# Kernel tuning notes

Measured on AMD Instinct MI355X. Metric: run time of the kernel, lower is better.

Reference implementation:

```python
import jax, jax.numpy as jnp
import numpy as np
import math

D_MODEL = 1024
N_HEADS = 16
D_HEAD = 64
D_MLP = 4096
N_LAYERS = 12
INIT_STD = 0.02
EPS = 1e-5
BATCH = 2
SEQ = 2048


def setup_inputs() -> dict:
    key = jax.random.key(0)
    ks = jax.random.split(key, 8)
    attn_std = INIT_STD
    proj_std = INIT_STD / math.sqrt(2 * N_LAYERS)
    return {
        "resid_pre": jax.random.normal(ks[0], (BATCH, SEQ, D_MODEL), jnp.float32),
        "ln1_w": jnp.ones((D_MODEL,), jnp.float32),
        "ln1_b": jnp.zeros((D_MODEL,), jnp.float32),
        "W_Q": attn_std * jax.random.normal(ks[1], (N_HEADS, D_MODEL, D_HEAD), jnp.float32),
        "b_Q": jnp.zeros((N_HEADS, D_HEAD), jnp.float32),
        "W_K": attn_std * jax.random.normal(ks[2], (N_HEADS, D_MODEL, D_HEAD), jnp.float32),
        "b_K": jnp.zeros((N_HEADS, D_HEAD), jnp.float32),
        "W_V": attn_std * jax.random.normal(ks[3], (N_HEADS, D_MODEL, D_HEAD), jnp.float32),
        "b_V": jnp.zeros((N_HEADS, D_HEAD), jnp.float32),
        "W_O": proj_std * jax.random.normal(ks[4], (N_HEADS, D_HEAD, D_MODEL), jnp.float32),
        "b_O": jnp.zeros((D_MODEL,), jnp.float32),
        "ln2_w": jnp.ones((D_MODEL,), jnp.float32),
        "ln2_b": jnp.zeros((D_MODEL,), jnp.float32),
        "W_in": INIT_STD * jax.random.normal(ks[5], (D_MODEL, D_MLP), jnp.float32),
        "b_in": jnp.zeros((D_MLP,), jnp.float32),
        "W_out": proj_std * jax.random.normal(ks[6], (D_MLP, D_MODEL), jnp.float32),
        "b_out": jnp.zeros((D_MODEL,), jnp.float32),
    }


def _layernorm(x, w, b):
    mean = x.mean(-1, keepdims=True)
    var = x.var(-1, keepdims=True)  # unbiased=False
    return (x - mean) / jnp.sqrt(var + EPS) * w + b


def _attention(x, W_Q, b_Q, W_K, b_K, W_V, b_V, W_O, b_O):
    # x: [b, s, d]; W_*: [h, d, k]
    q = jnp.einsum('bsd,hdk->bshk', x, W_Q) + b_Q
    k = jnp.einsum('bsd,hdk->bshk', x, W_K) + b_K
    v = jnp.einsum('bsd,hdk->bshk', x, W_V) + b_V
    scores = jnp.einsum('bqhk,bshk->bhqs', q, k) / math.sqrt(D_HEAD)
    seq = x.shape[1]
    causal = jnp.tril(jnp.ones((seq, seq), bool))
    scores = jnp.where(causal, scores, -jnp.inf)
    pattern = jax.nn.softmax(scores, axis=-1)
    z = jnp.einsum('bhqs,bshk->bqhk', pattern, v)
    return jnp.einsum('bqhk,hkd->bqd', z, W_O) + b_O


def reference(resid_pre, ln1_w, ln1_b, W_Q, b_Q, W_K, b_K, W_V, b_V, W_O, b_O,
              ln2_w, ln2_b, W_in, b_in, W_out, b_out):
    attn_out = _attention(_layernorm(resid_pre, ln1_w, ln1_b),
                          W_Q, b_Q, W_K, b_K, W_V, b_V, W_O, b_O)
    resid_mid = resid_pre + attn_out
    h = _layernorm(resid_mid, ln2_w, ln2_b)
    mlp_out = jnp.matmul(jax.nn.relu(jnp.matmul(h, W_in) + b_in), W_out) + b_out
    return resid_mid + mlp_out
```

## Files before the change

kernel.cpp:

```cpp
#include <hip/hip_runtime.h>
#include <stdint.h>


typedef unsigned short u16;
typedef __bf16 bf16x8 __attribute__((ext_vector_type(8)));
typedef __bf16 bf16x4 __attribute__((ext_vector_type(4)));
typedef short  s16x4  __attribute__((ext_vector_type(4)));
typedef float  f32x4  __attribute__((ext_vector_type(4)));

#define QSCALE 0.18033688011112042f

__device__ __forceinline__ float bf2f(unsigned int u) {
  union { unsigned int u; float f; } v; v.u = u << 16; return v.f;
}
__device__ __forceinline__ u16 f2bf(float f) {
  union { float f; unsigned int u; } v; v.f = f;
  unsigned int r = v.u + 0x7FFFu + ((v.u >> 16) & 1u);
  return (u16)(r >> 16);
}
__device__ __forceinline__ float loadf(const void* p, size_t i, int isf) {
  return isf ? ((const float*)p)[i] : bf2f(((const u16*)p)[i]);
}

typedef const __attribute__((address_space(1))) void* gas_t;
typedef __attribute__((address_space(3))) void* las_t;
__device__ __forceinline__ void gl_lds16(const u16* g, u16* l) {
  __builtin_amdgcn_global_load_lds((gas_t)g, (las_t)l, 16, 0, 0);
}

__device__ __forceinline__ f32x4 mfma16(s16x4 a, s16x4 b, f32x4 c) {
#if __has_builtin(__builtin_amdgcn_mfma_f32_16x16x16_bf16)
  return __builtin_amdgcn_mfma_f32_16x16x16_bf16(
      __builtin_bit_cast(bf16x4, a), __builtin_bit_cast(bf16x4, b), c, 0, 0, 0);
#else
  return __builtin_amdgcn_mfma_f32_16x16x16bf16_1k(a, b, c, 0, 0, 0);
#endif
}

__global__ __launch_bounds__(256) void detect_dtype(
    const unsigned int* __restrict__ x, int* __restrict__ flag) {
  __shared__ int cnt;
  if (threadIdx.x == 0) cnt = 0;
  __syncthreads();
  int c = 0;
  for (int i = threadIdx.x; i < 512; i += 256) {
    unsigned int e = (x[i] >> 23) & 0xFFu;
    if (e >= 97u && e <= 157u) c++;
  }
  atomicAdd(&cnt, c);
  __syncthreads();
  if (threadIdx.x == 0) *flag = (cnt > 384) ? 1 : 0;
}

__global__ __launch_bounds__(256) void pack_qkv_tiled(
    const int* __restrict__ flagp,
    const void* __restrict__ Wq, const void* __restrict__ Wk, const void* __restrict__ Wv,
    u16* __restrict__ WT) {
  __shared__ float t[64][65];
  const int isf = *flagp;
  const int tid = threadIdx.x;
  const int mh = blockIdx.y;
  const int mat = mh >> 4, h = mh & 15;
  const int d0 = blockIdx.x << 6;
  const void* src = (mat == 0) ? Wq : (mat == 1) ? Wk : Wv;
  const float scale = (mat == 0) ? QSCALE : 1.f;
  const int lane = tid & 63, rr = tid >> 6;
  const size_t sbase = ((size_t)h << 16) + lane;
#pragma unroll
  for (int i = 0; i < 16; i++) {
    int d = i * 4 + rr;
    t[d][lane] = loadf(src, sbase + (size_t)(d0 + d) * 64, isf) * scale;
  }
  __syncthreads();
#pragma unroll
  for (int i = 0; i < 16; i++) {
    int k = i * 4 + rr;
    WT[((size_t)((mat << 10) + (h << 6) + k) << 10) + d0 + lane] = f2bf(t[lane][k]);
  }
}

__global__ __launch_bounds__(256) void transpose_tiled(
    const int* __restrict__ flagp, const void* __restrict__ src,
    u16* __restrict__ dst, int R, int C) {
  __shared__ float t[64][65];
  const int isf = *flagp;
  const int tid = threadIdx.x;
  const int c0 = blockIdx.x << 6, r0 = blockIdx.y << 6;
  const int lane = tid & 63, rr = tid >> 6;
#pragma unroll
  for (int i = 0; i < 16; i++) {
    int r = i * 4 + rr;
    t[r][lane] = loadf(src, (size_t)(r0 + r) * C + c0 + lane, isf);
  }
  __syncthreads();
#pragma unroll
  for (int i = 0; i < 16; i++) {
    int c = i * 4 + rr;
    dst[(size_t)(c0 + c) * R + r0 + lane] = f2bf(t[lane][c]);
  }
}

__global__ __launch_bounds__(256) void pack_biases(
    const int* __restrict__ flagp,
    const void* bq, const void* bk, const void* bv,
    const void* bO, const void* bin, const void* bout,
    float* __restrict__ out) {
  const int isf = *flagp;
  int i = blockIdx.x * 256 + threadIdx.x;
  float v;
  if (i < 1024)      v = loadf(bq,   i,        isf) * QSCALE;
  else if (i < 2048) v = loadf(bk,   i - 1024, isf);
  else if (i < 3072) v = loadf(bv,   i - 2048, isf);
  else if (i < 4096) v = loadf(bO,   i - 3072, isf);
  else if (i < 8192) v = loadf(bin,  i - 4096, isf);
  else               v = loadf(bout, i - 8192, isf);
  out[i] = v;
}

template<int SRC>
__global__ __launch_bounds__(256) void ln_fwd(
    const int* __restrict__ flagp, const void* __restrict__ xin,
    const void* __restrict__ w, const void* __restrict__ b,
    u16* __restrict__ out) {
  const int isf = *flagp;
  const int row = blockIdx.x, tid = threadIdx.x;
  const int col = tid << 2;
  const size_t base = ((size_t)row << 10) + col;
  float v[4];
#pragma unroll
  for (int i = 0; i < 4; i++)
    v[i] = (SRC == 1) ? ((const float*)xin)[base + i] : loadf(xin, base + i, isf);
  float s  = v[0] + v[1] + v[2] + v[3];
  float ss = v[0]*v[0] + v[1]*v[1] + v[2]*v[2] + v[3]*v[3];
#pragma unroll
  for (int mk = 32; mk >= 1; mk >>= 1) {
    s  += __shfl_xor(s,  mk, 64);
    ss += __shfl_xor(ss, mk, 64);
  }
  __shared__ float red[8];
  if ((tid & 63) == 0) { red[tid >> 6] = s; red[4 + (tid >> 6)] = ss; }
  __syncthreads();
  float S  = red[0] + red[1] + red[2] + red[3];
  float SS = red[4] + red[5] + red[6] + red[7];
  float mean = S * (1.f / 1024.f);
  float var  = SS * (1.f / 1024.f) - mean * mean;
  float rstd = rsqrtf(var + 1e-5f);
  u16 e[4];
#pragma unroll
  for (int i = 0; i < 4; i++) {
    float wv = loadf(w, col + i, isf);
    float bv = loadf(b, col + i, isf);
    e[i] = f2bf((v[i] - mean) * rstd * wv + bv);
  }
  uint2 o;
  o.x = (unsigned)e[0] | ((unsigned)e[1] << 16);
  o.y = (unsigned)e[2] | ((unsigned)e[3] << 16);
  *(uint2*)(out + base) = o;
}

template<int MODE, int TM>
__global__ __launch_bounds__(256) void gemm_bt(
    const int* __restrict__ flagp,
    const u16* __restrict__ A, const u16* __restrict__ BT,
    const float* __restrict__ bias, const void* __restrict__ resid,
    void* __restrict__ out, void* __restrict__ out2, void* __restrict__ out3,
    int M, int N, int K, int SHL) {
  constexpr int WR = TM / 32;
  __shared__ u16 as[TM * 32];
  __shared__ u16 bs[128 * 32];
  int isf = 0;
  if (MODE == 2 || MODE == 3) isf = *flagp;
  const int Lb = blockIdx.x;
  const int xcd = Lb & 7, sidx = Lb >> 3;
  const int SH = 1 << SHL;
  const int by = xcd * SH + (sidx & (SH - 1));
  const int bx = sidx >> SHL;
  const int tid = threadIdx.x;
  const int L = tid & 63, w = tid >> 6;
  const int wm = (w >> 1) * (TM >> 1), wn = (w & 1) << 6;
  const int row0 = by * TM, col0 = bx << 7;
  const int m = L & 15, quad = L >> 4;

  f32x4 zero4 = {0.f, 0.f, 0.f, 0.f};
  f32x4 acc[WR][4];
#pragma unroll
  for (int i = 0; i < WR; i++)
#pragma unroll
    for (int j = 0; j < 4; j++) acc[i][j] = zero4;

  const int tm = tid >> 2;
  const int tk = (tid & 3) << 3;
  const u16* Ag  = A  + (size_t)(row0 + tm) * K + tk;
  const u16* Ag2 = Ag + (size_t)64 * K;
  const u16* Bg  = BT + (size_t)(col0 + tm) * K + tk;
  const u16* Bg2 = Bg + (size_t)64 * K;
  u16* asl  = &as[tid * 8];
  u16* asl2 = &as[2048 + tid * 8];
  u16* bsl  = &bs[tid * 8];
  u16* bsl2 = &bs[2048 + tid * 8];

  const int aoff = (wm + m) * 32 + quad * 8;
  const int boff = (wn + m) * 32 + quad * 8;

  for (int kk = 0; kk < K; kk += 32) {
    __syncthreads();
    gl_lds16(Ag + kk, asl);
    if (TM == 128) gl_lds16(Ag2 + kk, asl2);
    gl_lds16(Bg + kk, bsl);
    gl_lds16(Bg2 + kk, bsl2);
    __syncthreads();
    bf16x8 af[WR], bfr[4];
#pragma unroll
    for (int i = 0; i < WR; i++) af[i]  = *(const bf16x8*)&as[aoff + i * 512];
#pragma unroll
    for (int j = 0; j < 4; j++) bfr[j] = *(const bf16x8*)&bs[boff + j * 512];
#pragma unroll
    for (int i = 0; i < WR; i++)
#pragma unroll
      for (int j = 0; j < 4; j++)
        acc[i][j] = __builtin_amdgcn_mfma_f32_16x16x32_bf16(af[i], bfr[j], acc[i][j], 0, 0, 0);
  }

#pragma unroll
  for (int j = 0; j < 4; j++) {
    const int col = col0 + wn + j * 16 + m;
    const float bval = bias[col];
    if (MODE == 4) {
      const int sel = col >> 10;
      const int hh  = (col >> 6) & 15;
      const int f   = col & 63;
#pragma unroll
      for (int i = 0; i < WR; i++) {
        const int rowb = row0 + wm + i * 16 + quad * 4;
        if (sel < 2) {
          u16* dst = (u16*)(sel ? out2 : out);
#pragma unroll
          for (int r = 0; r < 4; r++)
            dst[((((size_t)hh << 12) + rowb + r) << 6) + f] = f2bf(acc[i][j][r] + bval);
        } else {
          u16 e[4];
#pragma unroll
          for (int r = 0; r < 4; r++) e[r] = f2bf(acc[i][j][r] + bval);
          uint2 o;
          o.x = (unsigned)e[0] | ((unsigned)e[1] << 16);
          o.y = (unsigned)e[2] | ((unsigned)e[3] << 16);
          *(uint2*)&((u16*)out3)[(((size_t)hh * 64 + f) << 12) + rowb] = o;
        }
      }
    } else {
#pragma unroll
      for (int i = 0; i < WR; i++) {
        const int rowb = row0 + wm + i * 16 + quad * 4;
#pragma unroll
        for (int r = 0; r < 4; r++) {
          float vv = acc[i][j][r] + bval;
          size_t idx = (size_t)(rowb + r) * N + col;
          if (MODE == 1) {
            ((u16*)out)[idx] = f2bf(fmaxf(vv, 0.f));
          } else if (MODE == 2) {
            ((float*)out)[idx] = vv + loadf(resid, idx, isf);
          } else if (MODE == 3) {
            float o = vv + ((const float*)resid)[idx];
            if (isf) ((float*)out)[idx] = o;
            else     ((u16*)out)[idx]   = f2bf(o);
          }
        }
      }
    }
  }
}

__global__ __launch_bounds__(256, 3) void attn_part(
    const u16* __restrict__ qh, const u16* __restrict__ kh,
    const u16* __restrict__ vT, u16* __restrict__ Opart,
    float* __restrict__ stats) {
  const int combo = blockIdx.x;
  const int qt = blockIdx.y;
  const int ci = blockIdx.z;
  const int q0 = qt << 6;
  const int nc = (q0 + 64 + 511) >> 9;
  if (ci >= nc) return;
  const int k_lo = ci << 9;
  const int k_hi = min(k_lo + 512, q0 + 64);
  const int nsteps = (k_hi - k_lo + 127) >> 7;

  __shared__ u16 kS[128 * 72];
  __shared__ u16 vS[64 * 136];
  const int tid = threadIdx.x, L = tid & 63, w = tid >> 6;
  const int m = L & 15, quad = L >> 4;
  const int h = combo >> 1, b = combo & 1;
  const size_t tb = (size_t)b * 2048;
  const size_t hbase = (size_t)h * 4096;
  const int qg = q0 + w * 16 + m;

  s16x4 qf[4];
  {
    const u16* qp = qh + ((hbase + tb + (size_t)(q0 + w * 16 + m)) << 6) + quad * 4;
#pragma unroll
    for (int fg = 0; fg < 4; fg++) qf[fg] = *(const s16x4*)(qp + fg * 16);
  }
  const s16x4 ones = {(short)0x3F80, (short)0x3F80, (short)0x3F80, (short)0x3F80};

  f32x4 zero4 = {0.f, 0.f, 0.f, 0.f};
  f32x4 O[4];
#pragma unroll
  for (int ft = 0; ft < 4; ft++) O[ft] = zero4;
  f32x4 lacc = zero4;
  float mrow = -30000.f;

  const int krow[4] = { (0*256+tid) >> 3, (1*256+tid) >> 3, (2*256+tid) >> 3, (3*256+tid) >> 3 };
  const int kc = tid & 7;
  const int vf[4] = { (0*256+tid) >> 4, (1*256+tid) >> 4, (2*256+tid) >> 4, (3*256+tid) >> 4 };
  const int vc = tid & 15;

  int4 kr[4], vr[4];
#pragma unroll
  for (int i = 0; i < 4; i++) {
    kr[i] = *(const int4*)(kh + ((hbase + tb + k_lo + krow[i]) << 6) + kc * 8);
    vr[i] = *(const int4*)(vT + (((size_t)h * 64 + vf[i]) << 12) + tb + k_lo + vc * 8);
  }

  for (int j = 0; j < nsteps; j++) {
    const int k0 = k_lo + (j << 7);
    __syncthreads();
#pragma unroll
    for (int i = 0; i < 4; i++) {
      *(int4*)&kS[krow[i] * 72 + kc * 8] = kr[i];
      *(int4*)&vS[vf[i] * 136 + vc * 8] = vr[i];
    }
    __syncthreads();
    if (j + 1 < nsteps) {
      const int k1 = k_lo + ((j + 1) << 7);
#pragma unroll
      for (int i = 0; i < 4; i++) {
        kr[i] = *(const int4*)(kh + ((hbase + tb + k1 + krow[i]) << 6) + kc * 8);
        vr[i] = *(const int4*)(vT + (((size_t)h * 64 + vf[i]) << 12) + tb + k1 + vc * 8);
      }
    }
    f32x4 sc[8];
#pragma unroll
    for (int kt = 0; kt < 8; kt++) {
      f32x4 t = zero4;
#pragma unroll
      for (int fg = 0; fg < 4; fg++) {
        s16x4 ka = *(const s16x4*)&kS[(kt * 16 + m) * 72 + fg * 16 + quad * 4];
        t = mfma16(ka, qf[fg], t);
      }
      sc[kt] = t;
    }
    if (k0 + 128 > q0) {
#pragma unroll
      for (int kt = 0; kt < 8; kt++)
#pragma unroll
        for (int r = 0; r < 4; r++) {
          int ktok = k0 + kt * 16 + quad * 4 + r;
          if (ktok > qg) sc[kt][r] = -30000.f;
        }
    }
    float mx = sc[0][0];
#pragma unroll
    for (int kt = 0; kt < 8; kt++)
#pragma unroll
      for (int r = 0; r < 4; r++) mx = fmaxf(mx, sc[kt][r]);
    mx = fmaxf(mx, __shfl_xor(mx, 16, 64));
    mx = fmaxf(mx, __shfl_xor(mx, 32, 64));
    float mnew = fmaxf(mrow, mx);
    float alpha = __builtin_amdgcn_exp2f(mrow - mnew);
    mrow = mnew;
#pragma unroll
    for (int ft = 0; ft < 4; ft++) O[ft] *= alpha;
    lacc *= alpha;
    s16x4 pb[8];
#pragma unroll
    for (int kt = 0; kt < 8; kt++)
#pragma unroll
      for (int r = 0; r < 4; r++)
        pb[kt][r] = (short)f2bf(__builtin_amdgcn_exp2f(sc[kt][r] - mnew));
#pragma unroll
    for (int kt = 0; kt < 8; kt++) {
      lacc = mfma16(ones, pb[kt], lacc);
#pragma unroll
      for (int ft = 0; ft < 4; ft++) {
        s16x4 va = *(const s16x4*)&vS[(ft * 16 + m) * 136 + kt * 16 + quad * 4];
        O[ft] = mfma16(va, pb[kt], O[ft]);
      }
    }
  }

  __syncthreads();
#pragma unroll
  for (int ft = 0; ft < 4; ft++) {
    s16x4 o4;
#pragma unroll
    for (int r = 0; r < 4; r++) o4[r] = (short)f2bf(O[ft][r]);
    *(s16x4*)&kS[(w * 16 + m) * 72 + ft * 16 + quad * 4] = o4;
  }
  __syncthreads();
  const int slot = (combo * 32 + qt) * 4 + ci;
  u16* op = Opart + ((size_t)slot << 12);
#pragma unroll
  for (int it = 0; it < 2; it++) {
    int idx = it * 256 + tid;
    int row = idx >> 3, c = idx & 7;
    *(int4*)&op[row * 64 + c * 8] = *(const int4*)&kS[row * 72 + c * 8];
  }
  if (quad == 0) {
    stats[slot * 128 + w * 16 + m]      = mrow;
    stats[slot * 128 + 64 + w * 16 + m] = lacc[0];
  }
}

__global__ __launch_bounds__(256) void attn_merge(
    const u16* __restrict__ Opart, const float* __restrict__ stats,
    u16* __restrict__ z) {
  const int combo = blockIdx.x, qt = blockIdx.y;
  const int h = combo >> 1, b = combo & 1;
  const int q0 = qt << 6;
  const int nc = (q0 + 64 + 511) >> 9;
  const int tid = threadIdx.x;
  const int t = tid >> 2, f0 = (tid & 3) << 4;
  const int slot0 = (combo * 32 + qt) * 4;
  float M = -3e4f;
  for (int ci = 0; ci < nc; ci++)
    M = fmaxf(M, stats[(slot0 + ci) * 128 + t]);
  float acc[16];
#pragma unroll
  for (int e = 0; e < 16; e++) acc[e] = 0.f;
  float ltot = 0.f;
  for (int ci = 0; ci < nc; ci++) {
    float mi = stats[(slot0 + ci) * 128 + t];
    float li = stats[(slot0 + ci) * 128 + 64 + t];
    float wgt = exp2f(mi - M);
    ltot += wgt * li;
    const u16* op = Opart + (((size_t)(slot0 + ci)) << 12) + t * 64 + f0;
    union { int4 v; u16 u[8]; } a0, a1;
    a0.v = *(const int4*)op;
    a1.v = *(const int4*)(op + 8);
#pragma unroll
    for (int e = 0; e < 8; e++) {
      acc[e]     += wgt * bf2f(a0.u[e]);
      acc[8 + e] += wgt * bf2f(a1.u[e]);
    }
  }
  float inv = 1.f / ltot;
  union { int4 v; u16 u[8]; } o0, o1;
#pragma unroll
  for (int e = 0; e < 8; e++) {
    o0.u[e] = f2bf(acc[e] * inv);
    o1.u[e] = f2bf(acc[8 + e] * inv);
  }
  size_t tok = (size_t)b * 2048 + q0 + t;
  *(int4*)&z[tok * 1024 + h * 64 + f0]     = o0.v;
  *(int4*)&z[tok * 1024 + h * 64 + f0 + 8] = o1.v;
}

extern "C" void kernel_launch(void* const* d_in, const int* in_sizes, int n_in,
                              void* d_out, int out_size, void* d_ws, size_t ws_size,
                              hipStream_t stream) {
  (void)in_sizes; (void)n_in; (void)out_size; (void)ws_size;
  const void* resid_pre = d_in[0];
  const void* ln1_w = d_in[1];
  const void* ln1_b = d_in[2];
  const void* W_Q   = d_in[3];
  const void* b_Q   = d_in[4];
  const void* W_K   = d_in[5];
  const void* b_K   = d_in[6];
  const void* W_V   = d_in[7];
  const void* b_V   = d_in[8];
  const void* W_O   = d_in[9];
  const void* b_O   = d_in[10];
  const void* ln2_w = d_in[11];
  const void* ln2_b = d_in[12];
  const void* W_in  = d_in[13];
  const void* b_in  = d_in[14];
  const void* W_out = d_in[15];
  const void* b_out = d_in[16];

  char* p = (char*)d_ws;
  auto alloc = [&](size_t bytes) {
    char* r = p; p += (bytes + 255) & ~(size_t)255; return (void*)r;
  };
  int*   flag      = (int*)  alloc(256);
  u16*   WqkvT     = (u16*)  alloc(3072ull * 1024 * 2);
  u16*   WoT       = (u16*)  alloc(1024ull * 1024 * 2);
  u16*   WinT      = (u16*)  alloc(4096ull * 1024 * 2);
  u16*   WoutT     = (u16*)  alloc(1024ull * 4096 * 2);
  float* biases    = (float*)alloc(9216 * 4);
  u16*   xn        = (u16*)  alloc(4096ull * 1024 * 2);
  u16*   q_hm      = (u16*)  alloc(16ull * 4096 * 64 * 2);
  u16*   k_hm      = (u16*)  alloc(16ull * 4096 * 64 * 2);
  u16*   vTws      = (u16*)  alloc(16ull * 64 * 4096 * 2);
  float* resid_mid = (float*)alloc(4096ull * 1024 * 4);
  u16*   h2        = (u16*)  alloc(4096ull * 1024 * 2);
  u16*   act       = (u16*)  alloc(4096ull * 4096 * 2);
  u16*   z = xn;
  u16*   Opart = act;
  float* stats = (float*)h2;

  detect_dtype<<<1, 256, 0, stream>>>((const unsigned int*)resid_pre, flag);

  pack_qkv_tiled<<<dim3(16, 48), 256, 0, stream>>>(flag, W_Q, W_K, W_V, WqkvT);
  transpose_tiled<<<dim3(16, 16), 256, 0, stream>>>(flag, W_O,   WoT,   1024, 1024);
  transpose_tiled<<<dim3(64, 16), 256, 0, stream>>>(flag, W_in,  WinT,  1024, 4096);
  transpose_tiled<<<dim3(16, 64), 256, 0, stream>>>(flag, W_out, WoutT, 4096, 1024);
  pack_biases<<<36, 256, 0, stream>>>(flag, b_Q, b_K, b_V, b_O, b_in, b_out, biases);

  ln_fwd<0><<<4096, 256, 0, stream>>>(flag, resid_pre, ln1_w, ln1_b, xn);
  gemm_bt<4, 128><<<768, 256, 0, stream>>>(
      flag, xn, WqkvT, biases, nullptr, q_hm, k_hm, vTws, 4096, 3072, 1024, 2);
  attn_part<<<dim3(32, 32, 4), 256, 0, stream>>>(q_hm, k_hm, vTws, Opart, stats);
  attn_merge<<<dim3(32, 32), 256, 0, stream>>>(Opart, stats, z);
  gemm_bt<2, 64><<<512, 256, 0, stream>>>(
      flag, z, WoT, biases + 3072, resid_pre, resid_mid, nullptr, nullptr, 4096, 1024, 1024, 3);
  ln_fwd<1><<<4096, 256, 0, stream>>>(flag, resid_mid, ln2_w, ln2_b, h2);
  gemm_bt<1, 128><<<1024, 256, 0, stream>>>(
      flag, h2, WinT, biases + 4096, nullptr, act, nullptr, nullptr, 4096, 4096, 1024, 2);
  gemm_bt<3, 64><<<512, 256, 0, stream>>>(
      flag, act, WoutT, biases + 8192, resid_mid, d_out, nullptr, nullptr, 4096, 1024, 4096, 3);
}
```

Before: 498.6 us.

## Rework attention MFMA shapes, row-sum, V layout, and GEMM register prefetch

The GEMM drops direct global-to-LDS loads in favour of register double-buffering: the next K tile is fetched into registers while MFMAs run on the current one. The attention QK^T now uses 16x16x32 bf16 MFMAs with 8-wide loads. The row-sum moves from an MFMA against a ones vector to scalar adds plus shuffles. V is stored into LDS with a permuted column layout so PV operands can be read as 8-wide vectors. Float-to-bf16 conversions use the packed hardware convert when available. These changes aim to cut instruction count and LDS traffic, at the cost of more registers and a riskier layout change.

```diff
diff --git a/kernel.cpp b/kernel.cpp
--- a/kernel.cpp
+++ b/kernel.cpp
@@ -5,6 +5,7 @@
 typedef unsigned short u16;
 typedef __bf16 bf16x8 __attribute__((ext_vector_type(8)));
 typedef __bf16 bf16x4 __attribute__((ext_vector_type(4)));
+typedef __bf16 bf16x2 __attribute__((ext_vector_type(2)));
 typedef short  s16x4  __attribute__((ext_vector_type(4)));
 typedef float  f32x4  __attribute__((ext_vector_type(4)));
 
@@ -18,14 +19,16 @@
   unsigned int r = v.u + 0x7FFFu + ((v.u >> 16) & 1u);
   return (u16)(r >> 16);
 }
+__device__ __forceinline__ unsigned pkbf(float lo, float hi) {
+#if __has_builtin(__builtin_amdgcn_cvt_pk_bf16_f32)
+  bf16x2 t = __builtin_amdgcn_cvt_pk_bf16_f32(lo, hi);
+  return __builtin_bit_cast(unsigned, t);
+#else
+  return (unsigned)f2bf(lo) | ((unsigned)f2bf(hi) << 16);
+#endif
+}
 __device__ __forceinline__ float loadf(const void* p, size_t i, int isf) {
   return isf ? ((const float*)p)[i] : bf2f(((const u16*)p)[i]);
-}
-
-typedef const __attribute__((address_space(1))) void* gas_t;
-typedef __attribute__((address_space(3))) void* las_t;
-__device__ __forceinline__ void gl_lds16(const u16* g, u16* l) {
-  __builtin_amdgcn_global_load_lds((gas_t)g, (las_t)l, 16, 0, 0);
 }
 
 __device__ __forceinline__ f32x4 mfma16(s16x4 a, s16x4 b, f32x4 c) {
@@ -202,13 +205,25 @@
   const int aoff = (wm + m) * 32 + quad * 8;
   const int boff = (wn + m) * 32 + quad * 8;
 
+  int4 ar0, ar1, br0, br1;
+  ar0 = *(const int4*)Ag;
+  if (TM == 128) ar1 = *(const int4*)Ag2;
+  br0 = *(const int4*)Bg;
+  br1 = *(const int4*)Bg2;
+
   for (int kk = 0; kk < K; kk += 32) {
     __syncthreads();
-    gl_lds16(Ag + kk, asl);
-    if (TM == 128) gl_lds16(Ag2 + kk, asl2);
-    gl_lds16(Bg + kk, bsl);
-    gl_lds16(Bg2 + kk, bsl2);
+    *(int4*)asl = ar0;
+    if (TM == 128) *(int4*)asl2 = ar1;
+    *(int4*)bsl = br0;
+    *(int4*)bsl2 = br1;
     __syncthreads();
+    if (kk + 32 < K) {
+      ar0 = *(const int4*)(Ag + kk + 32);
+      if (TM == 128) ar1 = *(const int4*)(Ag2 + kk + 32);
+      br0 = *(const int4*)(Bg + kk + 32);
+      br1 = *(const int4*)(Bg2 + kk + 32);
+    }
     bf16x8 af[WR], bfr[4];
 #pragma unroll
     for (int i = 0; i < WR; i++) af[i]  = *(const bf16x8*)&as[aoff + i * 512];
@@ -238,12 +253,9 @@
           for (int r = 0; r < 4; r++)
             dst[((((size_t)hh << 12) + rowb + r) << 6) + f] = f2bf(acc[i][j][r] + bval);
         } else {
-          u16 e[4];
-#pragma unroll
-          for (int r = 0; r < 4; r++) e[r] = f2bf(acc[i][j][r] + bval);
           uint2 o;
-          o.x = (unsigned)e[0] | ((unsigned)e[1] << 16);
-          o.y = (unsigned)e[2] | ((unsigned)e[3] << 16);
+          o.x = pkbf(acc[i][j][0] + bval, acc[i][j][1] + bval);
+          o.y = pkbf(acc[i][j][2] + bval, acc[i][j][3] + bval);
           *(uint2*)&((u16*)out3)[(((size_t)hh * 64 + f) << 12) + rowb] = o;
         }
       }
@@ -293,25 +305,27 @@
   const size_t hbase = (size_t)h * 4096;
   const int qg = q0 + w * 16 + m;
 
-  s16x4 qf[4];
+  bf16x8 qb0, qb1;
   {
-    const u16* qp = qh + ((hbase + tb + (size_t)(q0 + w * 16 + m)) << 6) + quad * 4;
-#pragma unroll
-    for (int fg = 0; fg < 4; fg++) qf[fg] = *(const s16x4*)(qp + fg * 16);
-  }
-  const s16x4 ones = {(short)0x3F80, (short)0x3F80, (short)0x3F80, (short)0x3F80};
+    const u16* qp = qh + ((hbase + tb + (size_t)qg) << 6) + quad * 8;
+    qb0 = *(const bf16x8*)qp;
+    qb1 = *(const bf16x8*)(qp + 32);
+  }
 
   f32x4 zero4 = {0.f, 0.f, 0.f, 0.f};
   f32x4 O[4];
 #pragma unroll
   for (int ft = 0; ft < 4; ft++) O[ft] = zero4;
-  f32x4 lacc = zero4;
-  float mrow = -30000.f;
+  float mrow = -30000.f, lrow = 0.f;
 
   const int krow[4] = { (0*256+tid) >> 3, (1*256+tid) >> 3, (2*256+tid) >> 3, (3*256+tid) >> 3 };
   const int kc = tid & 7;
   const int vf[4] = { (0*256+tid) >> 4, (1*256+tid) >> 4, (2*256+tid) >> 4, (3*256+tid) >> 4 };
   const int vc = tid & 15;
+  const int vq = (vc & 1) << 1;
+  const int vk4 = (vc >> 1) << 2;
+  const int vc0 = (vq << 5) + vk4;
+  const int vc1 = ((vq + 1) << 5) + vk4;
 
   int4 kr[4], vr[4];
 #pragma unroll
@@ -326,7 +340,9 @@
 #pragma unroll
     for (int i = 0; i < 4; i++) {
       *(int4*)&kS[krow[i] * 72 + kc * 8] = kr[i];
-      *(int4*)&vS[vf[i] * 136 + vc * 8] = vr[i];
+      union { int4 v; s16x4 hh[2]; } tv; tv.v = vr[i];
+      *(s16x4*)&vS[vf[i] * 136 + vc0] = tv.hh[0];
+      *(s16x4*)&vS[vf[i] * 136 + vc1] = tv.hh[1];
     }
     __syncthreads();
     if (j + 1 < nsteps) {
@@ -340,12 +356,12 @@
     f32x4 sc[8];
 #pragma unroll
     for (int kt = 0; kt < 8; kt++) {
+      const u16* kp = &kS[(kt * 16 + m) * 72 + quad * 8];
+      bf16x8 ka0 = *(const bf16x8*)kp;
+      bf16x8 ka1 = *(const bf16x8*)(kp + 32);
       f32x4 t = zero4;
-#pragma unroll
-      for (int fg = 0; fg < 4; fg++) {
-        s16x4 ka = *(const s16x4*)&kS[(kt * 16 + m) * 72 + fg * 16 + quad * 4];
-        t = mfma16(ka, qf[fg], t);
-      }
+      t = __builtin_amdgcn_mfma_f32_16x16x32_bf16(ka0, qb0, t, 0, 0, 0);
+      t = __builtin_amdgcn_mfma_f32_16x16x32_bf16(ka1, qb1, t, 0, 0, 0);
       sc[kt] = t;
     }
     if (k0 + 128 > q0) {
@@ -367,22 +383,34 @@
     float mnew = fmaxf(mrow, mx);
     float alpha = __builtin_amdgcn_exp2f(mrow - mnew);
     mrow = mnew;
+    s16x4 pb[8];
+    float sum = 0.f;
+#pragma unroll
+    for (int kt = 0; kt < 8; kt++) {
+      float e0 = __builtin_amdgcn_exp2f(sc[kt][0] - mnew);
+      float e1 = __builtin_amdgcn_exp2f(sc[kt][1] - mnew);
+      float e2 = __builtin_amdgcn_exp2f(sc[kt][2] - mnew);
+      float e3 = __builtin_amdgcn_exp2f(sc[kt][3] - mnew);
+      sum += (e0 + e1) + (e2 + e3);
+      union { uint2 u; s16x4 hh; } pu;
+      pu.u.x = pkbf(e0, e1);
+      pu.u.y = pkbf(e2, e3);
+      pb[kt] = pu.hh;
+    }
+    sum += __shfl_xor(sum, 16, 64);
+    sum += __shfl_xor(sum, 32, 64);
+    lrow = lrow * alpha + sum;
 #pragma unroll
     for (int ft = 0; ft < 4; ft++) O[ft] *= alpha;
-    lacc *= alpha;
-    s16x4 pb[8];
-#pragma unroll
-    for (int kt = 0; kt < 8; kt++)
-#pragma unroll
-      for (int r = 0; r < 4; r++)
-        pb[kt][r] = (short)f2bf(__builtin_amdgcn_exp2f(sc[kt][r] - mnew));
-#pragma unroll
-    for (int kt = 0; kt < 8; kt++) {
-      lacc = mfma16(ones, pb[kt], lacc);
-#pragma unroll
-      for (int ft = 0; ft < 4; ft++) {
-        s16x4 va = *(const s16x4*)&vS[(ft * 16 + m) * 136 + kt * 16 + quad * 4];
-        O[ft] = mfma16(va, pb[kt], O[ft]);
+#pragma unroll
+    for (int ft = 0; ft < 4; ft++) {
+      const u16* vp = &vS[(ft * 16 + m) * 136 + quad * 32];
+#pragma unroll
+      for (int pr = 0; pr < 4; pr++) {
+        union { bf16x8 v; s16x4 hh[2]; } u;
+        u.v = *(const bf16x8*)(vp + pr * 8);
+        O[ft] = mfma16(u.hh[0], pb[2 * pr],     O[ft]);
+        O[ft] = mfma16(u.hh[1], pb[2 * pr + 1], O[ft]);
       }
     }
   }
@@ -390,10 +418,10 @@
   __syncthreads();
 #pragma unroll
   for (int ft = 0; ft < 4; ft++) {
-    s16x4 o4;
-#pragma unroll
-    for (int r = 0; r < 4; r++) o4[r] = (short)f2bf(O[ft][r]);
-    *(s16x4*)&kS[(w * 16 + m) * 72 + ft * 16 + quad * 4] = o4;
+    union { uint2 u; s16x4 hh; } o4;
+    o4.u.x = pkbf(O[ft][0], O[ft][1]);
+    o4.u.y = pkbf(O[ft][2], O[ft][3]);
+    *(s16x4*)&kS[(w * 16 + m) * 72 + ft * 16 + quad * 4] = o4.hh;
   }
   __syncthreads();
   const int slot = (combo * 32 + qt) * 4 + ci;
@@ -406,7 +434,7 @@
   }
   if (quad == 0) {
     stats[slot * 128 + w * 16 + m]      = mrow;
-    stats[slot * 128 + 64 + w * 16 + m] = lacc[0];
+    stats[slot * 128 + 64 + w * 16 + m] = lrow;
   }
 }
 
```

Result: faster. 432.6 us (-13.2%).
